# Kernel tuning notes

Hardware: AMD Instinct MI355X
Metric: run time of the kernel (lower is better)

The kernel has to match this reference:

```python
import jax, jax.numpy as jnp
import numpy as np

CONF_THRESH = 0.01
TOP_K = 200        # per-class NMS candidate cap
NMS_THRESH = 0.45
KEEP_TOP_K = 200   # global per-image cap; also output K
TEMPERATURE = 1.0
V0, V1 = 0.1, 0.2  # variances


def _nms_keep(bxs, scs):
    """Greedy NMS over candidates sorted descending by score.
    bxs: [M,4] (x1,y1,x2,y2), scs: [M] (invalid slots have score -1).
    Returns keep mask [M] (bool). Matches torch nm_suppression: a box j is
    suppressed by kept box i iff NOT (IoU(i,j) <= thresh) (NaN IoU suppresses)."""
    x1, y1, x2, y2 = bxs[:, 0], bxs[:, 1], bxs[:, 2], bxs[:, 3]
    area = (x2 - x1) * (y2 - y1)
    xx1 = jnp.maximum(x1[:, None], x1[None, :])
    yy1 = jnp.maximum(y1[:, None], y1[None, :])
    xx2 = jnp.minimum(x2[:, None], x2[None, :])
    yy2 = jnp.minimum(y2[:, None], y2[None, :])
    inter = jnp.clip(xx2 - xx1, 0.0) * jnp.clip(yy2 - yy1, 0.0)
    union = area[None, :] - inter + area[:, None]  # row i: area[i] + area[j] - inter
    iou = inter / union  # [M,M]
    M = scs.shape[0]
    valid = scs > CONF_THRESH

    def step(active, i):
        k_i = active[i]                                  # kept iff still active (sorted desc)
        sup = k_i & jnp.logical_not(iou[i] <= NMS_THRESH)
        return active & jnp.logical_not(sup), k_i

    _, keep = jax.lax.scan(step, valid, jnp.arange(M))
    return keep


def _forward(loc_data, conf_data, dbox_list):
    B, N, C = conf_data.shape
    M, K = TOP_K, KEEP_TOP_K
    # --- box decode (SSD) ---
    db = dbox_list[None]                                   # [1,N,4]
    cxcy = db[..., :2] + loc_data[..., :2] * V0 * db[..., 2:]
    wh = db[..., 2:] * jnp.exp(loc_data[..., 2:] * V1)
    mins = cxcy - wh * 0.5
    boxes = jnp.clip(jnp.concatenate([mins, mins + wh], -1), 0.0, 1.0)  # [B,N,4]
    # --- class scores ---
    probs = jax.nn.softmax(conf_data / TEMPERATURE, axis=-1)
    sc = jnp.swapaxes(probs[..., 1:], 1, 2)                # [B,C-1,N] (skip background)
    masked = jnp.where(sc > CONF_THRESH, sc, -1.0)
    top_sc, top_idx = jax.lax.top_k(masked, M)             # [B,C-1,M] desc
    cand = jnp.take_along_axis(boxes[:, None], top_idx[..., None], axis=2)  # [B,C-1,M,4]
    # --- per-class greedy NMS ---
    keep = jax.vmap(jax.vmap(_nms_keep))(cand, top_sc)     # [B,C-1,M]
    kept_sc = jnp.where(keep, top_sc, 0.0)
    # --- global keep_top_k across classes (torch topk over concatenated dets) ---
    flat = kept_sc.reshape(B, -1)
    order = jnp.argsort(-flat, axis=1)
    rank = jnp.argsort(order, axis=1)                      # inverse permutation = desc rank
    keep_g = (flat > 0.0) & (rank < K)
    fin_sc = jnp.where(keep_g, flat, 0.0).reshape(B, C - 1, M)
    fin_bx = jnp.where(keep_g.reshape(B, C - 1, M)[..., None], cand, 0.0)
    # --- per-class compaction (stable desc sort keeps NMS order among survivors) ---
    ord2 = jnp.argsort(-fin_sc, axis=2)
    sc_out = jnp.take_along_axis(fin_sc, ord2, axis=2)[..., :K]
    bx_out = jnp.take_along_axis(fin_bx, ord2[..., None], axis=2)[..., :K, :]
    body = jnp.concatenate([sc_out[..., None], bx_out], axis=-1)  # [B,C-1,K,5]
    bg = jnp.zeros((B, 1, K, 5), body.dtype)               # class 0 (background) row stays 0
    return jnp.concatenate([bg, body], axis=1)             # [B,C,K,5]


def setup_inputs() -> dict:
    key = jax.random.key(0)
    k1, k2, k3 = jax.random.split(key, 3)
    B, N, C = 8, 32768, 81
    loc_data = jax.random.normal(k1, (B, N, 4), jnp.float32)
    conf_data = jax.random.normal(k2, (B, N, C), jnp.float32)
    dbox_list = jax.random.uniform(k3, (N, 4), jnp.float32, 0.05, 0.95)  # cx,cy,w,h priors
    return {"loc_data": loc_data, "conf_data": conf_data, "dbox_list": dbox_list}


def reference(loc_data, conf_data, dbox_list):
    return _forward(loc_data, conf_data, dbox_list)
```

## Files before the change

kernel.cpp:

```cpp
#include <hip/hip_runtime.h>
#include <stdint.h>

#define CONF_T 0.01f
#define NMS_T  0.45f
#define M_TOP  200
#define TK_BS  512
#define NMS_BS 256
#define TCAP   2048

typedef float float4u __attribute__((ext_vector_type(4), aligned(4)));

__device__ __forceinline__ uint32_t fkey(float f) {
    uint32_t u = __float_as_uint(f);
    return (u & 0x80000000u) ? ~u : (u | 0x80000000u);
}
__device__ __forceinline__ float fkey_inv(uint32_t k) {
    uint32_t u = (k & 0x80000000u) ? (k & 0x7FFFFFFFu) : ~k;
    return __uint_as_float(u);
}

__device__ __forceinline__ void suffix_select(
        uint32_t* hist, uint32_t* wsum, int nb, uint32_t pref, int shift,
        uint32_t wantv, uint32_t* s_prefix, uint32_t* s_want) {
    int tid = threadIdx.x;
    int lane = tid & 63, w = tid >> 6;
    int bpt = nb >> 8;
    int base = tid * bpt;
    uint32_t loc = 0, sfx = 0;
    if (tid < 256) {
        for (int j = 0; j < bpt; j++) loc += hist[base + j];
        sfx = loc;
        #pragma unroll
        for (int d = 1; d < 64; d <<= 1) {
            uint32_t y = __shfl_down(sfx, d);
            if (lane + d < 64) sfx += y;
        }
        if (lane == 0) wsum[w] = sfx;
    }
    __syncthreads();
    if (tid < 256) {
        uint32_t later = 0;
        for (int j = w + 1; j < 4; j++) later += wsum[j];
        uint32_t run = (sfx - loc) + later;
        for (int j = bpt - 1; j >= 0; j--) {
            uint32_t h = hist[base + j];
            uint32_t s2 = run + h;
            if (run < wantv && s2 >= wantv) {
                *s_prefix = pref | ((uint32_t)(base + j) << shift);
                *s_want   = wantv - run;
            }
            run = s2;
        }
    }
    __syncthreads();
}

__device__ __forceinline__ void suffix_select2(
        uint32_t* hist, uint32_t* wsum, int nb, uint32_t want_a, uint32_t want_b,
        uint32_t* s_bin_a, uint32_t* s_bin_b) {
    int tid = threadIdx.x;
    int lane = tid & 63, w = tid >> 6;
    int bpt = nb >> 8;
    int base = tid * bpt;
    uint32_t loc = 0, sfx = 0;
    if (tid < 256) {
        for (int j = 0; j < bpt; j++) loc += hist[base + j];
        sfx = loc;
        #pragma unroll
        for (int d = 1; d < 64; d <<= 1) {
            uint32_t y = __shfl_down(sfx, d);
            if (lane + d < 64) sfx += y;
        }
        if (lane == 0) wsum[w] = sfx;
    }
    __syncthreads();
    if (tid < 256) {
        uint32_t later = 0;
        for (int j = w + 1; j < 4; j++) later += wsum[j];
        uint32_t run = (sfx - loc) + later;
        for (int j = bpt - 1; j >= 0; j--) {
            uint32_t h = hist[base + j];
            uint32_t s2 = run + h;
            if (run < want_a && s2 >= want_a) *s_bin_a = (uint32_t)(base + j);
            if (run < want_b && s2 >= want_b) *s_bin_b = (uint32_t)(base + j);
            run = s2;
        }
    }
    __syncthreads();
}

__device__ __forceinline__ float4 decode_box(float4 l, float4 d) {
    float cx = d.x + (l.x * 0.1f) * d.z;
    float cy = d.y + (l.y * 0.1f) * d.w;
    float w  = d.z * expf(l.z * 0.2f);
    float h  = d.w * expf(l.w * 0.2f);
    float x1 = cx - w * 0.5f, y1 = cy - h * 0.5f;
    float x2 = x1 + w, y2 = y1 + h;
    float4 o;
    o.x = fminf(fmaxf(x1, 0.f), 1.f);
    o.y = fminf(fmaxf(y1, 0.f), 1.f);
    o.z = fminf(fmaxf(x2, 0.f), 1.f);
    o.w = fminf(fmaxf(y2, 0.f), 1.f);
    return o;
}

__global__ __launch_bounds__(256, 4) void softmax_kernel(
        const float* __restrict__ conf, float* __restrict__ sc,
        int* __restrict__ pcnt, int B, int N, int C) {
    int r = blockIdx.x * blockDim.x + threadIdx.x;
    if (r < B) pcnt[r] = 0;
    if (r >= B * N) return;
    const float* p = conf + (size_t)r * 81;
    float v[81];
    #pragma unroll
    for (int i = 0; i < 20; i++) {
        float4u f = *(const float4u*)(p + 4 * i);
        v[4 * i] = f.x; v[4 * i + 1] = f.y; v[4 * i + 2] = f.z; v[4 * i + 3] = f.w;
    }
    v[80] = p[80];
    float m = v[0];
    #pragma unroll
    for (int c = 1; c < 81; c++) m = fmaxf(m, v[c]);
    float s = 0.f;
    #pragma unroll
    for (int c = 0; c < 81; c++) { float e = expf(v[c] - m); v[c] = e; s += e; }
    int b = r / N, n = r % N;
    float* obase = sc + ((size_t)b * (C - 1)) * N + n;
    #pragma unroll
    for (int c = 1; c < 81; c++) obase[(size_t)(c - 1) * N] = v[c] / s;
}

__global__ __launch_bounds__(TK_BS) void sel_kernel(
        const float* __restrict__ sc,
        float* __restrict__ tval, int* __restrict__ tidx,
        int B, int N, int Cm1) {
    const uint32_t KEYN1 = 0x407FFFFFu;
    const uint32_t BIN_N1 = KEYN1 >> 21;
    __shared__ __align__(16) uint32_t hist[2048];
    __shared__ __align__(16) uint32_t tk[TCAP];
    __shared__ int      tix[TCAP];
    __shared__ uint32_t wsum[4];
    __shared__ uint32_t s_prefix, s_want, s_bin_a, s_bin_b;
    __shared__ uint32_t ngt, ntie, tcnt;
    __shared__ float    e_val[256];
    __shared__ int      e_idx[256];
    __shared__ int      tiebuf[256];

    int row = blockIdx.x;
    int tid = threadIdx.x;
    const float* v = sc + (size_t)row * N;
    const float4* v4 = (const float4*)v;
    int n4 = N >> 2;

    bool sampled = (N >= 2048) && ((N & 3) == 0);
    float loF = 0.f, hiF = 0.f;
    if (sampled) {
        int stride = N >> 2;
        float smp[4];
        #pragma unroll
        for (int s = 0; s < 4; s++) smp[s] = v[s * stride + tid];
        for (int i = tid; i < 2048; i += TK_BS) hist[i] = 0;
        __syncthreads();
        #pragma unroll
        for (int s = 0; s < 4; s++) {
            float f = smp[s];
            atomicAdd(&hist[fkey(f > CONF_T ? f : -1.0f) >> 21], 1u);
        }
        __syncthreads();
        suffix_select2(hist, wsum, 2048, 3u, 25u, &s_bin_a, &s_bin_b);
        uint32_t h = s_bin_a, l = s_bin_b;
        uint32_t hi_key = ((h + 1) << 21) - 1u;
        uint32_t lo_key = (l << 21) - 1u;
        hiF = fkey_inv(hi_key);
        loF = fmaxf(fkey_inv(lo_key), CONF_T);
        sampled = (l > BIN_N1);
    }

    if (tid < 256) { e_val[tid] = -1.0f; e_idx[tid] = tid; }
    if (tid == 0) { ngt = 0; ntie = 0; tcnt = 0; }
    __syncthreads();

    bool ok = false;
    uint32_t G = 0, T = 0;
    if (sampled) {
        for (int i0 = tid; i0 < n4; i0 += 16 * TK_BS) {
            float4 f[16];
            #pragma unroll
            for (int u = 0; u < 16; u++) {
                int i = i0 + u * TK_BS;
                if (i < n4) f[u] = v4[i];
            }
            #pragma unroll
            for (int u = 0; u < 16; u++) {
                int i = i0 + u * TK_BS;
                if (i < n4) {
                    float e[4] = { f[u].x, f[u].y, f[u].z, f[u].w };
                    #pragma unroll
                    for (int j = 0; j < 4; j++) {
                        float fv = e[j];
                        if (fv > loF) {
                            int idx = 4 * i + j;
                            if (fv > hiF) {
                                uint32_t p = atomicAdd(&ngt, 1u);
                                if (p < 256) { e_val[p] = fv; e_idx[p] = idx; }
                            } else {
                                uint32_t p = atomicAdd(&tcnt, 1u);
                                if (p < TCAP) { tk[p] = fkey(fv); tix[p] = idx; }
                            }
                        }
                    }
                }
            }
        }
        for (int i = (n4 << 2) + tid; i < N; i += TK_BS) {
            float fv = v[i];
            if (fv > loF) {
                if (fv > hiF) {
                    uint32_t p = atomicAdd(&ngt, 1u);
                    if (p < 256) { e_val[p] = fv; e_idx[p] = i; }
                } else {
                    uint32_t p = atomicAdd(&tcnt, 1u);
                    if (p < TCAP) { tk[p] = fkey(fv); tix[p] = i; }
                }
            }
        }
        __syncthreads();
        G = ngt; T = tcnt;
        ok = (G <= (uint32_t)M_TOP) && (T <= (uint32_t)TCAP) &&
             (G + T >= (uint32_t)M_TOP);
    }

    uint32_t kth = KEYN1, rfin = 0;
    if (ok) {
        uint32_t want_t = (uint32_t)M_TOP - G;
        if (want_t > 0) {
            for (int i = tid; i < 2048; i += TK_BS) hist[i] = 0;
            __syncthreads();
            for (int i = tid; i < (int)T; i += TK_BS) atomicAdd(&hist[tk[i] >> 21], 1u);
            __syncthreads();
            suffix_select(hist, wsum, 2048, 0u, 21, want_t, &s_prefix, &s_want);
            uint32_t pre0 = s_prefix, w0 = s_want;
            uint32_t bb0 = pre0 >> 21;
            for (int i = tid; i < 2048; i += TK_BS) hist[i] = 0;
            __syncthreads();
            for (int i = tid; i < (int)T; i += TK_BS)
                if ((tk[i] >> 21) == bb0) atomicAdd(&hist[(tk[i] >> 10) & 2047u], 1u);
            __syncthreads();
            suffix_select(hist, wsum, 2048, pre0, 10, w0, &s_prefix, &s_want);
            uint32_t pre1 = s_prefix, w1 = s_want;
            for (int i = tid; i < 1024; i += TK_BS) hist[i] = 0;
            __syncthreads();
            for (int i = tid; i < (int)T; i += TK_BS)
                if ((tk[i] >> 10) == (pre1 >> 10)) atomicAdd(&hist[tk[i] & 1023u], 1u);
            __syncthreads();
            suffix_select(hist, wsum, 1024, pre1, 0, w1, &s_prefix, &s_want);
            kth = s_prefix; rfin = s_want;
            for (int i = tid; i < (int)T; i += TK_BS) {
                uint32_t k = tk[i];
                if (k > kth) {
                    uint32_t p = atomicAdd(&ngt, 1u);
                    if (p < 256) { e_val[p] = fkey_inv(k); e_idx[p] = tix[i]; }
                } else if (k == kth) {
                    uint32_t p = atomicAdd(&ntie, 1u);
                    if (p < 256) tiebuf[p] = tix[i];
                }
            }
            __syncthreads();
        }
    } else {
        if (tid < 256) { e_val[tid] = -1.0f; e_idx[tid] = tid; }
        if (tid == 0) { ngt = 0; ntie = 0; tcnt = 0; }
        for (int i = tid; i < 2048; i += TK_BS) hist[i] = 0;
        __syncthreads();
        for (int i = tid; i < n4; i += TK_BS) {
            float4 f = v4[i];
            atomicAdd(&hist[fkey(f.x > CONF_T ? f.x : -1.0f) >> 21], 1u);
            atomicAdd(&hist[fkey(f.y > CONF_T ? f.y : -1.0f) >> 21], 1u);
            atomicAdd(&hist[fkey(f.z > CONF_T ? f.z : -1.0f) >> 21], 1u);
            atomicAdd(&hist[fkey(f.w > CONF_T ? f.w : -1.0f) >> 21], 1u);
        }
        for (int i = (n4 << 2) + tid; i < N; i += TK_BS)
            atomicAdd(&hist[fkey(v[i] > CONF_T ? v[i] : -1.0f) >> 21], 1u);
        __syncthreads();
        suffix_select(hist, wsum, 2048, 0u, 21, M_TOP, &s_prefix, &s_want);
        uint32_t b0 = s_prefix >> 21;
        uint32_t want1 = s_want;
        bool collect_ties = (b0 != BIN_N1);
        for (int i = tid; i < N; i += TK_BS) {
            float f = v[i];
            float mv = f > CONF_T ? f : -1.0f;
            uint32_t k = fkey(mv);
            uint32_t bin = k >> 21;
            if (bin > b0) {
                uint32_t p = atomicAdd(&ngt, 1u);
                if (p < 256) { e_val[p] = mv; e_idx[p] = i; }
            } else if (bin == b0 && collect_ties) {
                uint32_t p = atomicAdd(&tcnt, 1u);
                if (p < TCAP) { tk[p] = k; tix[p] = i; }
            }
        }
        __syncthreads();
        if (collect_ties && tcnt <= TCAP) {
            int Tl = (int)tcnt;
            for (int i = tid; i < 2048; i += TK_BS) hist[i] = 0;
            __syncthreads();
            for (int i = tid; i < Tl; i += TK_BS) atomicAdd(&hist[(tk[i] >> 10) & 2047u], 1u);
            __syncthreads();
            suffix_select(hist, wsum, 2048, b0 << 21, 10, want1, &s_prefix, &s_want);
            uint32_t pre2 = s_prefix; uint32_t want2 = s_want;
            uint32_t b1 = (pre2 >> 10) & 2047u;
            for (int i = tid; i < 1024; i += TK_BS) hist[i] = 0;
            __syncthreads();
            for (int i = tid; i < Tl; i += TK_BS)
                if (((tk[i] >> 10) & 2047u) == b1) atomicAdd(&hist[tk[i] & 1023u], 1u);
            __syncthreads();
            suffix_select(hist, wsum, 1024, pre2, 0, want2, &s_prefix, &s_want);
            kth = s_prefix; rfin = s_want;
            for (int i = tid; i < Tl; i += TK_BS) {
                uint32_t k = tk[i];
                if (k > kth) {
                    uint32_t p = atomicAdd(&ngt, 1u);
                    if (p < 256) { e_val[p] = fkey_inv(k); e_idx[p] = tix[i]; }
                } else if (k == kth) {
                    uint32_t p = atomicAdd(&ntie, 1u);
                    if (p < 256) tiebuf[p] = tix[i];
                }
            }
            __syncthreads();
        } else if (collect_ties) {
            const int shifts[2] = {10, 0};
            const int nbins_[2] = {2048, 1024};
            if (tid == 0) { s_prefix = b0 << 21; s_want = want1; }
            __syncthreads();
            for (int lev = 0; lev < 2; lev++) {
                int shift = shifts[lev];
                int nb = nbins_[lev];
                uint32_t bmask = (uint32_t)nb - 1u;
                uint32_t pref = s_prefix, wantv = s_want;
                uint32_t pmask = 0xFFFFFFFFu << (shift + ((nb == 2048) ? 11 : 10));
                for (int i = tid; i < nb; i += TK_BS) hist[i] = 0;
                __syncthreads();
                for (int i = tid; i < N; i += TK_BS) {
                    float f = v[i];
                    uint32_t k = fkey(f > CONF_T ? f : -1.0f);
                    if ((k & pmask) == (pref & pmask)) atomicAdd(&hist[(k >> shift) & bmask], 1u);
                }
                __syncthreads();
                suffix_select(hist, wsum, nb, pref, shift, wantv, &s_prefix, &s_want);
            }
            kth = s_prefix; rfin = s_want;
            for (int i = tid; i < N; i += TK_BS) {
                float f = v[i];
                float mv = f > CONF_T ? f : -1.0f;
                uint32_t k = fkey(mv);
                if ((k >> 21) == b0) {
                    if (k > kth) {
                        uint32_t p = atomicAdd(&ngt, 1u);
                        if (p < 256) { e_val[p] = mv; e_idx[p] = i; }
                    } else if (k == kth) {
                        uint32_t p = atomicAdd(&ntie, 1u);
                        if (p < 256) tiebuf[p] = i;
                    }
                }
            }
            __syncthreads();
        }
    }

    uint32_t gcount = min(ngt, (uint32_t)M_TOP);
    uint32_t nt = min(ntie, 256u);
    if (tid < (int)nt) {
        int mine = tiebuf[tid];
        uint32_t rk = 0;
        for (uint32_t j = 0; j < nt; j++) if (tiebuf[j] < mine) rk++;
        if (rk < rfin) {
            uint32_t slot = gcount + rk;
            if (slot < M_TOP) { e_val[slot] = fkey_inv(kth); e_idx[slot] = mine; }
        }
    }
    __syncthreads();
    uint64_t* e_pack = (uint64_t*)tk;
    if (tid < 256)
        e_pack[tid] = ((uint64_t)fkey(e_val[tid]) << 32) | (uint32_t)~(uint32_t)e_idx[tid];
    __syncthreads();
    if (tid < M_TOP) {
        uint64_t mine = e_pack[tid];
        uint32_t rk = 0;
        for (int j = 0; j < M_TOP; j++) rk += (e_pack[j] > mine) ? 1u : 0u;
        tval[(size_t)row * M_TOP + rk] = e_val[tid];
        tidx[(size_t)row * M_TOP + rk] = e_idx[tid];
    }
}

__global__ __launch_bounds__(NMS_BS) void nms_kernel(
        const float* __restrict__ tval, const int* __restrict__ tidx,
        const float* __restrict__ loc, const float* __restrict__ dbox,
        float* __restrict__ cand,
        float* __restrict__ cmpval, int* __restrict__ cmpidx,
        int* __restrict__ pcnt,
        int B, int N, int Cm1, int M) {
    __shared__ __align__(16) float4 s_bb[M_TOP];
    __shared__ float    s_ar[M_TOP];
    __shared__ float    s_sc[M_TOP];
    __shared__ __align__(16) uint64_t supT[M_TOP * 4];

    int row = blockIdx.x;
    int b = row / Cm1, c = row % Cm1;
    int tid = threadIdx.x;

    if (tid < M_TOP) {
        float mv = tval[(size_t)row * M_TOP + tid];
        int   mi = tidx[(size_t)row * M_TOP + tid];
        float4 l = ((const float4*)loc)[(size_t)b * N + mi];
        float4 d = ((const float4*)dbox)[mi];
        float4 bx = decode_box(l, d);
        ((float4*)cand)[(size_t)row * M_TOP + tid] = bx;
        s_sc[tid] = mv;
        s_bb[tid] = bx;
        s_ar[tid] = (bx.z - bx.x) * (bx.w - bx.y);
    }
    __syncthreads();

    for (int t = tid; t < M_TOP * 4; t += NMS_BS) {
        int iw = t / M_TOP;
        int j  = t - iw * M_TOP;
        float4 bj = s_bb[j];
        float arJ = s_ar[j];
        int i0 = iw << 6;
        int iN = M_TOP - i0; if (iN > 64) iN = 64; if (iN < 0) iN = 0;
        uint64_t m = 0;
        for (int k = 0; k < iN; k++) {
            float4 bi = s_bb[i0 + k];
            float xx1 = fmaxf(bi.x, bj.x);
            float yy1 = fmaxf(bi.y, bj.y);
            float xx2 = fminf(bi.z, bj.z);
            float yy2 = fminf(bi.w, bj.w);
            float inter = fmaxf(xx2 - xx1, 0.f) * fmaxf(yy2 - yy1, 0.f);
            float uni = (arJ - inter) + s_ar[i0 + k];
            float iou = inter / uni;
            if (!(iou <= NMS_T)) m |= (1ull << k);
        }
        supT[(j << 2) + iw] = m;
    }
    __syncthreads();

    if (tid < 64) {
        int lane = tid;
        uint64_t st0[4], st1[4], st2[4], st3[4];
        bool alive[4]; int keepb[4];
        #pragma unroll
        for (int s = 0; s < 4; s++) {
            int j = (s << 6) + lane;
            bool inb = (j < M_TOP);
            uint64_t w0 = inb ? supT[(j << 2) + 0] : 0ull;
            uint64_t w1 = inb ? supT[(j << 2) + 1] : 0ull;
            uint64_t w2 = inb ? supT[(j << 2) + 2] : 0ull;
            uint64_t w3 = inb ? supT[(j << 2) + 3] : 0ull;
            if (s == 0) { st0[0]=w0; st0[1]=w1; st0[2]=w2; st0[3]=w3; }
            if (s == 1) { st1[0]=w0; st1[1]=w1; st1[2]=w2; st1[3]=w3; }
            if (s == 2) { st2[0]=w0; st2[1]=w1; st2[2]=w2; st2[3]=w3; }
            if (s == 3) { st3[0]=w0; st3[1]=w1; st3[2]=w2; st3[3]=w3; }
            alive[s] = inb ? (s_sc[j] > CONF_T) : false;
            keepb[s] = 0;
        }
        #pragma unroll
        for (int iw = 0; iw < 4; iw++) {
            int lim = M_TOP - (iw << 6); if (lim > 64) lim = 64; if (lim < 0) lim = 0;
            for (int b2 = 0; b2 < lim; b2++) {
                uint64_t mask = __ballot(alive[iw]);
                if ((mask >> b2) & 1ull) {
                    if (lane == b2) keepb[iw] = 1;
                    alive[0] = alive[0] && !((st0[iw] >> b2) & 1ull);
                    alive[1] = alive[1] && !((st1[iw] >> b2) & 1ull);
                    alive[2] = alive[2] && !((st2[iw] >> b2) & 1ull);
                    alive[3] = alive[3] && !((st3[iw] >> b2) & 1ull);
                }
            }
        }
        unsigned long long ball[4];
        int total = 0;
        #pragma unroll
        for (int s = 0; s < 4; s++) { ball[s] = __ballot(keepb[s] != 0); total += (int)__popcll(ball[s]); }
        int base = 0;
        if (lane == 0 && total > 0) base = atomicAdd(&pcnt[b], total);
        base = __shfl(base, 0);
        unsigned long long lower = (lane == 0) ? 0ull : (~0ull >> (64 - lane));
        int off = base;
        #pragma unroll
        for (int s = 0; s < 4; s++) {
            if (keepb[s]) {
                int pos = off + (int)__popcll(ball[s] & lower);
                cmpval[(size_t)b * M + pos] = s_sc[(s << 6) + lane];
                cmpidx[(size_t)b * M + pos] = c * M_TOP + (s << 6) + lane;
            }
            off += (int)__popcll(ball[s]);
        }
    }
}

#define GT_BS 1024
__global__ __launch_bounds__(GT_BS) void gtop_kernel(
        const float* __restrict__ cmpval, const int* __restrict__ cmpidx,
        const int* __restrict__ pcnt, float* __restrict__ gl_val,
        int* __restrict__ gl_idx, int* __restrict__ gl_cnt, int M) {
    int b = blockIdx.x;
    int tid = threadIdx.x;
    int P = pcnt[b];
    const float* cv = cmpval + (size_t)b * M;
    const int*   ci = cmpidx + (size_t)b * M;
    if (P <= M_TOP) {
        for (int i = tid; i < P; i += GT_BS) {
            gl_val[b * M_TOP + i] = cv[i];
            gl_idx[b * M_TOP + i] = ci[i];
        }
        if (tid == 0) gl_cnt[b] = P;
        return;
    }
    __shared__ uint32_t hist[256];
    __shared__ uint32_t s_prefix, s_want;
    __shared__ int tiebuf[256];
    __shared__ uint32_t ntie, wcnt;
    __shared__ int cutoff;
    if (tid == 0) { s_prefix = 0; s_want = M_TOP; }
    for (int pass = 0; pass < 4; pass++) {
        if (tid < 256) hist[tid] = 0;
        __syncthreads();
        uint32_t prefix = s_prefix;
        int shift = 24 - 8 * pass;
        for (int i = tid; i < P; i += GT_BS) {
            uint32_t k = fkey(cv[i]);
            bool ok = (pass == 0) || ((k >> (shift + 8)) == (prefix >> (shift + 8)));
            if (ok) atomicAdd(&hist[(k >> shift) & 255u], 1u);
        }
        __syncthreads();
        if (tid == 0) {
            uint32_t want = s_want, cum = 0; int bin = 0;
            for (int bb = 255; bb >= 0; bb--) {
                if (cum + hist[bb] >= want) { bin = bb; break; }
                cum += hist[bb];
            }
            s_want = want - cum;
            s_prefix = prefix | ((uint32_t)bin << shift);
        }
        __syncthreads();
    }
    uint32_t kth = s_prefix, rfin = s_want;
    if (tid == 0) { ntie = 0; cutoff = -1; wcnt = 0; }
    __syncthreads();
    for (int i = tid; i < P; i += GT_BS) {
        if (fkey(cv[i]) == kth) { uint32_t p = atomicAdd(&ntie, 1u); if (p < 256) tiebuf[p] = ci[i]; }
    }
    __syncthreads();
    uint32_t nt = min(ntie, 256u);
    if (tid < (int)nt) {
        int mine = tiebuf[tid];
        uint32_t rk = 0;
        for (uint32_t j = 0; j < nt; j++) if (tiebuf[j] < mine) rk++;
        if (rk == rfin - 1) cutoff = mine;
    }
    __syncthreads();
    int cut = cutoff;
    for (int i = tid; i < P; i += GT_BS) {
        uint32_t k = fkey(cv[i]);
        if (k > kth || (k == kth && ci[i] <= cut)) {
            uint32_t p = atomicAdd(&wcnt, 1u);
            gl_val[b * M_TOP + p] = cv[i];
            gl_idx[b * M_TOP + p] = ci[i];
        }
    }
    if (tid == 0) gl_cnt[b] = M_TOP;
}

__global__ __launch_bounds__(256) void out_kernel(
        const float* __restrict__ gl_val, const int* __restrict__ gl_idx,
        const int* __restrict__ gl_cnt, const float* __restrict__ cand,
        float* __restrict__ out, int C, int Cm1) {
    int row = blockIdx.x;
    int b = row / C, cc = row % C;
    int tid = threadIdx.x;
    size_t oslab = (size_t)row * M_TOP * 5;
    if (cc == 0) {
        float4 z; z.x = 0.f; z.y = 0.f; z.z = 0.f; z.w = 0.f;
        float4* o4 = (float4*)(out + oslab);
        for (int i = tid; i < M_TOP * 5 / 4; i += 256) o4[i] = z;
        return;
    }
    int c = cc - 1;
    __shared__ float lv[M_TOP];
    __shared__ int   lm[M_TOP];
    __shared__ uint32_t nloc;
    if (tid == 0) nloc = 0;
    __syncthreads();
    int cnt = gl_cnt[b];
    for (int i = tid; i < cnt; i += 256) {
        int idx = gl_idx[b * M_TOP + i];
        if (idx / M_TOP == c) {
            uint32_t p = atomicAdd(&nloc, 1u);
            lv[p] = gl_val[b * M_TOP + i];
            lm[p] = idx % M_TOP;
        }
    }
    __syncthreads();
    int nc = (int)nloc;
    if (tid < M_TOP) {
        if (tid < nc) {
            float v = lv[tid]; int m = lm[tid];
            int rk = 0;
            for (int j = 0; j < nc; j++)
                if (lv[j] > v || (lv[j] == v && lm[j] < m)) rk++;
            float4 bb = ((const float4*)cand)[((size_t)(b * Cm1 + c)) * M_TOP + m];
            size_t o = oslab + (size_t)rk * 5;
            out[o] = v; out[o + 1] = bb.x; out[o + 2] = bb.y;
            out[o + 3] = bb.z; out[o + 4] = bb.w;
        } else {
            size_t o = oslab + (size_t)tid * 5;
            out[o] = 0.f; out[o + 1] = 0.f; out[o + 2] = 0.f;
            out[o + 3] = 0.f; out[o + 4] = 0.f;
        }
    }
}

extern "C" void kernel_launch(void* const* d_in, const int* in_sizes, int n_in,
                              void* d_out, int out_size, void* d_ws, size_t ws_size,
                              hipStream_t stream) {
    const float* loc  = (const float*)d_in[0];
    const float* conf = (const float*)d_in[1];
    const float* dbox = (const float*)d_in[2];
    int N   = in_sizes[2] / 4;
    int B   = in_sizes[0] / (4 * N);
    int C   = in_sizes[1] / (B * N);
    int Cm1 = C - 1;
    int M   = Cm1 * M_TOP;

    char* ws = (char*)d_ws;
    size_t off = 0;
    auto alloc = [&](size_t bytes) -> char* {
        char* p = ws + off;
        off = (off + bytes + 255) & ~(size_t)255;
        return p;
    };
    float* sc     = (float*)alloc((size_t)B * Cm1 * N * sizeof(float));
    float* cand   = (float*)alloc((size_t)B * M * 4 * sizeof(float));
    int*   pcnt   = (int*)alloc((size_t)B * sizeof(int));
    float* cmpval = (float*)alloc((size_t)B * M * sizeof(float));
    int*   cmpidx = (int*)alloc((size_t)B * M * sizeof(int));
    float* gl_val = (float*)alloc((size_t)B * M_TOP * sizeof(float));
    int*   gl_idx = (int*)alloc((size_t)B * M_TOP * sizeof(int));
    int*   gl_cnt = (int*)alloc((size_t)B * sizeof(int));
    float* tval   = (float*)alloc((size_t)B * Cm1 * M_TOP * sizeof(float));
    int*   tidx   = (int*)alloc((size_t)B * Cm1 * M_TOP * sizeof(int));

    int bn = B * N;
    softmax_kernel<<<(bn + 255) / 256, 256, 0, stream>>>(conf, sc, pcnt, B, N, C);
    sel_kernel<<<B * Cm1, TK_BS, 0, stream>>>(sc, tval, tidx, B, N, Cm1);
    nms_kernel<<<B * Cm1, NMS_BS, 0, stream>>>(tval, tidx, loc, dbox, cand,
                                               cmpval, cmpidx, pcnt, B, N, Cm1, M);
    gtop_kernel<<<B, GT_BS, 0, stream>>>(cmpval, cmpidx, pcnt, gl_val, gl_idx, gl_cnt, M);
    out_kernel<<<B * C, 256, 0, stream>>>(gl_val, gl_idx, gl_cnt, cand, (float*)d_out, C, Cm1);
}
```

Measured before the change: 278.7 us.

## Replace materialized softmax+per-class top-k with sampled-threshold streaming selection

Instead of writing the full [B,C-1,N] softmax matrix and running a radix select over each row, the code samples 2048 anchors per image to estimate per-class score thresholds. It then streams conf once, recomputing softmax and using a log-domain quick reject to collect only candidates above the threshold into small per-row buffers. A finish kernel resolves the exact top-200 from those buffers and falls back to a full recompute when the estimate fails. The NMS IoU mask now computes only the lower-triangular entries, and gtop uses the parallel suffix_select. The aim is to remove the large score-matrix write and re-read, at the cost of added complexity, atomics and a slow fallback path.

```diff
diff --git a/kernel.cpp b/kernel.cpp
--- a/kernel.cpp
+++ b/kernel.cpp
@@ -6,7 +6,11 @@
 #define M_TOP  200
 #define TK_BS  512
 #define NMS_BS 256
+#define FIN_BS 512
 #define TCAP   2048
+#define GCAP   256
+#define KEYN1  0x407FFFFFu
+#define BIN_N1 (KEYN1 >> 21)
 
 typedef float float4u __attribute__((ext_vector_type(4), aligned(4)));
 
@@ -24,7 +28,7 @@
         uint32_t wantv, uint32_t* s_prefix, uint32_t* s_want) {
     int tid = threadIdx.x;
     int lane = tid & 63, w = tid >> 6;
-    int bpt = nb >> 8;
+    int bpt = nb >> 8; if (bpt < 1) bpt = 1;
     int base = tid * bpt;
     uint32_t loc = 0, sfx = 0;
     if (tid < 256) {
@@ -104,6 +108,356 @@
     return o;
 }
 
+__device__ __forceinline__ void softmax_ms(const float* __restrict__ p,
+                                           float& m_out, float& s_out) {
+    float m;
+    {
+        float4u f = *(const float4u*)p;
+        m = f.x; m = fmaxf(m, f.y); m = fmaxf(m, f.z); m = fmaxf(m, f.w);
+        #pragma unroll
+        for (int i = 1; i < 20; i++) {
+            float4u g = *(const float4u*)(p + 4 * i);
+            m = fmaxf(m, g.x); m = fmaxf(m, g.y); m = fmaxf(m, g.z); m = fmaxf(m, g.w);
+        }
+        m = fmaxf(m, p[80]);
+    }
+    float s = 0.f;
+    #pragma unroll
+    for (int i = 0; i < 20; i++) {
+        float4u g = *(const float4u*)(p + 4 * i);
+        s += expf(g.x - m); s += expf(g.y - m); s += expf(g.z - m); s += expf(g.w - m);
+    }
+    s += expf(p[80] - m);
+    m_out = m; s_out = s;
+}
+
+__global__ __launch_bounds__(256) void samp_kernel(
+        const float* __restrict__ conf, float* __restrict__ samp, int N, int Cm1) {
+    int b = blockIdx.x >> 3;
+    int t = ((blockIdx.x & 7) << 8) + threadIdx.x;
+    int n = (t >> 9) * (N >> 2) + (t & 511);
+    const float* p = conf + ((size_t)b * N + n) * 81;
+    float m, s; softmax_ms(p, m, s);
+    float* ob = samp + ((size_t)b * Cm1) * 2048 + t;
+    #pragma unroll
+    for (int i = 0; i < 20; i++) {
+        float4u g = *(const float4u*)(p + 4 * i);
+        float e4[4] = { g.x, g.y, g.z, g.w };
+        #pragma unroll
+        for (int j = 0; j < 4; j++) {
+            int c = 4 * i + j;
+            if (c >= 1) ob[(size_t)(c - 1) * 2048] = expf(e4[j] - m) / s;
+        }
+    }
+    ob[(size_t)(Cm1 - 1) * 2048] = expf(p[80] - m) / s;
+}
+
+__global__ __launch_bounds__(TK_BS) void thr_kernel(
+        const float* __restrict__ samp, float* __restrict__ thrLo,
+        float* __restrict__ thrHi, uint32_t* __restrict__ gcnt,
+        uint32_t* __restrict__ tcnt, int* __restrict__ pcnt, int Cm1) {
+    __shared__ uint32_t hist[2048];
+    __shared__ uint32_t wsum[4];
+    __shared__ uint32_t s_bin_a, s_bin_b;
+    int row = blockIdx.x, tid = threadIdx.x;
+    const float* sp = samp + ((size_t)row << 11);
+    for (int i = tid; i < 2048; i += TK_BS) hist[i] = 0;
+    __syncthreads();
+    for (int i = tid; i < 2048; i += TK_BS) {
+        float f = sp[i];
+        atomicAdd(&hist[fkey(f > CONF_T ? f : -1.0f) >> 21], 1u);
+    }
+    __syncthreads();
+    suffix_select2(hist, wsum, 2048, 3u, 25u, &s_bin_a, &s_bin_b);
+    if (tid == 0) {
+        uint32_t h = s_bin_a, l = s_bin_b;
+        uint32_t hi_key = ((h + 1) << 21) - 1u;
+        uint32_t lo_key = (l << 21) - 1u;
+        float hiF = fkey_inv(hi_key);
+        float loF = fmaxf(fkey_inv(lo_key), CONF_T);
+        bool rok = (l > BIN_N1);
+        thrLo[row] = rok ? loF : __uint_as_float(0x7F800000u);
+        thrHi[row] = hiF;
+        gcnt[row] = 0; tcnt[row] = 0;
+        if ((row % Cm1) == 0) pcnt[row / Cm1] = 0;
+    }
+}
+
+__global__ __launch_bounds__(256) void fsel_kernel(
+        const float* __restrict__ conf,
+        const float* __restrict__ thrLo, const float* __restrict__ thrHi,
+        float* __restrict__ gval, int* __restrict__ gidx, uint32_t* __restrict__ gcnt,
+        uint32_t* __restrict__ tkey, int* __restrict__ tixg, uint32_t* __restrict__ tcnt,
+        int N, int Cm1) {
+    __shared__ float s_lo[128], s_hi[128], s_ln[128];
+    int nb = N >> 8;
+    int b = blockIdx.x / nb;
+    int n = ((blockIdx.x % nb) << 8) + threadIdx.x;
+    if (threadIdx.x < Cm1) {
+        float lo = thrLo[b * Cm1 + threadIdx.x];
+        s_lo[threadIdx.x] = lo;
+        s_hi[threadIdx.x] = thrHi[b * Cm1 + threadIdx.x];
+        s_ln[threadIdx.x] = logf(lo);
+    }
+    __syncthreads();
+    const float* p = conf + ((size_t)b * N + n) * 81;
+    float m, s; softmax_ms(p, m, s);
+    float t0m = m + logf(s) - 1e-3f;
+    int lane = threadIdx.x & 63;
+    uint64_t lowerm = (lane == 0) ? 0ull : (~0ull >> (64 - lane));
+    int rowb = b * Cm1;
+
+    auto proc = [&](int c, float x) {
+        bool quick = x > (t0m + s_ln[c - 1]);
+        uint64_t mq = __ballot(quick);
+        if (mq == 0) return;
+        float fv = 0.f; bool ex = false, hb = false;
+        if (quick) {
+            fv = expf(x - m) / s;
+            ex = fv > s_lo[c - 1];
+            hb = ex && (fv > s_hi[c - 1]);
+        }
+        uint64_t mhi = __ballot(hb);
+        uint64_t mlo = __ballot(ex && !hb);
+        int row = rowb + (c - 1);
+        if (mhi) {
+            int src = (int)__ffsll((unsigned long long)mhi) - 1;
+            uint32_t bse = 0;
+            if (lane == src) bse = atomicAdd(&gcnt[row], (uint32_t)__popcll(mhi));
+            bse = (uint32_t)__shfl((int)bse, src);
+            if (hb) {
+                uint32_t pp = bse + (uint32_t)__popcll(mhi & lowerm);
+                if (pp < GCAP) {
+                    gval[(size_t)row * GCAP + pp] = fv;
+                    gidx[(size_t)row * GCAP + pp] = n;
+                }
+            }
+        }
+        if (mlo) {
+            int src = (int)__ffsll((unsigned long long)mlo) - 1;
+            uint32_t bse = 0;
+            if (lane == src) bse = atomicAdd(&tcnt[row], (uint32_t)__popcll(mlo));
+            bse = (uint32_t)__shfl((int)bse, src);
+            if (ex && !hb) {
+                uint32_t pp = bse + (uint32_t)__popcll(mlo & lowerm);
+                if (pp < TCAP) {
+                    tkey[(size_t)row * TCAP + pp] = fkey(fv);
+                    tixg[(size_t)row * TCAP + pp] = n;
+                }
+            }
+        }
+    };
+
+    {
+        float4u g = *(const float4u*)p;
+        proc(1, g.y); proc(2, g.z); proc(3, g.w);
+    }
+    for (int i = 1; i < 20; i++) {
+        float4u g = *(const float4u*)(p + 4 * i);
+        proc(4 * i, g.x); proc(4 * i + 1, g.y); proc(4 * i + 2, g.z); proc(4 * i + 3, g.w);
+    }
+    proc(80, p[80]);
+}
+
+__global__ __launch_bounds__(FIN_BS) void fin_kernel(
+        const float* __restrict__ conf,
+        const float* __restrict__ thrLo,
+        const float* __restrict__ gval, const int* __restrict__ gidx,
+        const uint32_t* __restrict__ gcnt,
+        const uint32_t* __restrict__ tkeyg, const int* __restrict__ tixg2,
+        const uint32_t* __restrict__ tcntg,
+        float* __restrict__ tval, int* __restrict__ tidx,
+        int N, int Cm1) {
+    __shared__ __align__(16) uint32_t hist[2048];
+    __shared__ __align__(16) uint32_t tk[TCAP];
+    __shared__ int      tix[TCAP];
+    __shared__ uint32_t wsum[4];
+    __shared__ uint32_t s_prefix, s_want;
+    __shared__ uint32_t ngt, ntie, tcs;
+    __shared__ float    e_val[256];
+    __shared__ int      e_idx[256];
+    __shared__ int      tiebuf[256];
+
+    int row = blockIdx.x, tid = threadIdx.x;
+    int b = row / Cm1, cls = (row % Cm1) + 1;
+    uint32_t G = gcnt[row], T = tcntg[row];
+    bool ok = (thrLo[row] < 2.0f) && (G <= (uint32_t)M_TOP) &&
+              (T <= (uint32_t)TCAP) && (G + T >= (uint32_t)M_TOP);
+
+    if (tid < 256) { e_val[tid] = -1.0f; e_idx[tid] = tid; }
+    if (tid == 0) { ngt = 0; ntie = 0; tcs = 0; }
+    __syncthreads();
+
+    uint32_t kth = KEYN1, rfin = 0;
+    if (ok) {
+        if (tid < (int)G) {
+            e_val[tid] = gval[(size_t)row * GCAP + tid];
+            e_idx[tid] = gidx[(size_t)row * GCAP + tid];
+        }
+        for (int i = tid; i < (int)T; i += FIN_BS) {
+            tk[i]  = tkeyg[(size_t)row * TCAP + i];
+            tix[i] = tixg2[(size_t)row * TCAP + i];
+        }
+        if (tid == 0) ngt = G;
+        __syncthreads();
+        uint32_t want_t = (uint32_t)M_TOP - G;
+        if (want_t > 0) {
+            for (int i = tid; i < 2048; i += FIN_BS) hist[i] = 0;
+            __syncthreads();
+            for (int i = tid; i < (int)T; i += FIN_BS) atomicAdd(&hist[tk[i] >> 21], 1u);
+            __syncthreads();
+            suffix_select(hist, wsum, 2048, 0u, 21, want_t, &s_prefix, &s_want);
+            uint32_t pre0 = s_prefix, w0 = s_want;
+            uint32_t bb0 = pre0 >> 21;
+            for (int i = tid; i < 2048; i += FIN_BS) hist[i] = 0;
+            __syncthreads();
+            for (int i = tid; i < (int)T; i += FIN_BS)
+                if ((tk[i] >> 21) == bb0) atomicAdd(&hist[(tk[i] >> 10) & 2047u], 1u);
+            __syncthreads();
+            suffix_select(hist, wsum, 2048, pre0, 10, w0, &s_prefix, &s_want);
+            uint32_t pre1 = s_prefix, w1 = s_want;
+            for (int i = tid; i < 1024; i += FIN_BS) hist[i] = 0;
+            __syncthreads();
+            for (int i = tid; i < (int)T; i += FIN_BS)
+                if ((tk[i] >> 10) == (pre1 >> 10)) atomicAdd(&hist[tk[i] & 1023u], 1u);
+            __syncthreads();
+            suffix_select(hist, wsum, 1024, pre1, 0, w1, &s_prefix, &s_want);
+            kth = s_prefix; rfin = s_want;
+            for (int i = tid; i < (int)T; i += FIN_BS) {
+                uint32_t k = tk[i];
+                if (k > kth) {
+                    uint32_t pq = atomicAdd(&ngt, 1u);
+                    if (pq < 256) { e_val[pq] = fkey_inv(k); e_idx[pq] = tix[i]; }
+                } else if (k == kth) {
+                    uint32_t pq = atomicAdd(&ntie, 1u);
+                    if (pq < 256) tiebuf[pq] = tix[i];
+                }
+            }
+            __syncthreads();
+        }
+    } else {
+        auto probf = [&](int i) -> float {
+            const float* pp = conf + ((size_t)b * N + i) * 81;
+            float mm, ss; softmax_ms(pp, mm, ss);
+            return expf(pp[cls] - mm) / ss;
+        };
+        for (int i = tid; i < 2048; i += FIN_BS) hist[i] = 0;
+        __syncthreads();
+        for (int i = tid; i < N; i += FIN_BS) {
+            float f = probf(i);
+            atomicAdd(&hist[fkey(f > CONF_T ? f : -1.0f) >> 21], 1u);
+        }
+        __syncthreads();
+        suffix_select(hist, wsum, 2048, 0u, 21, (uint32_t)M_TOP, &s_prefix, &s_want);
+        uint32_t b0 = s_prefix >> 21;
+        uint32_t want1 = s_want;
+        bool collect = (b0 != BIN_N1);
+        for (int i = tid; i < N; i += FIN_BS) {
+            float f = probf(i);
+            float mv = f > CONF_T ? f : -1.0f;
+            uint32_t k = fkey(mv);
+            uint32_t bin = k >> 21;
+            if (bin > b0) {
+                uint32_t pq = atomicAdd(&ngt, 1u);
+                if (pq < 256) { e_val[pq] = mv; e_idx[pq] = i; }
+            } else if (bin == b0 && collect) {
+                uint32_t pq = atomicAdd(&tcs, 1u);
+                if (pq < TCAP) { tk[pq] = k; tix[pq] = i; }
+            }
+        }
+        __syncthreads();
+        if (collect && tcs <= TCAP) {
+            int Tl = (int)tcs;
+            for (int i = tid; i < 2048; i += FIN_BS) hist[i] = 0;
+            __syncthreads();
+            for (int i = tid; i < Tl; i += FIN_BS) atomicAdd(&hist[(tk[i] >> 10) & 2047u], 1u);
+            __syncthreads();
+            suffix_select(hist, wsum, 2048, b0 << 21, 10, want1, &s_prefix, &s_want);
+            uint32_t pre2 = s_prefix, want2 = s_want;
+            uint32_t b1 = (pre2 >> 10) & 2047u;
+            for (int i = tid; i < 1024; i += FIN_BS) hist[i] = 0;
+            __syncthreads();
+            for (int i = tid; i < Tl; i += FIN_BS)
+                if (((tk[i] >> 10) & 2047u) == b1) atomicAdd(&hist[tk[i] & 1023u], 1u);
+            __syncthreads();
+            suffix_select(hist, wsum, 1024, pre2, 0, want2, &s_prefix, &s_want);
+            kth = s_prefix; rfin = s_want;
+            for (int i = tid; i < Tl; i += FIN_BS) {
+                uint32_t k = tk[i];
+                if (k > kth) {
+                    uint32_t pq = atomicAdd(&ngt, 1u);
+                    if (pq < 256) { e_val[pq] = fkey_inv(k); e_idx[pq] = tix[i]; }
+                } else if (k == kth) {
+                    uint32_t pq = atomicAdd(&ntie, 1u);
+                    if (pq < 256) tiebuf[pq] = tix[i];
+                }
+            }
+            __syncthreads();
+        } else if (collect) {
+            const int shifts[2] = {10, 0};
+            const int nbins_[2] = {2048, 1024};
+            if (tid == 0) { s_prefix = b0 << 21; s_want = want1; }
+            __syncthreads();
+            for (int lev = 0; lev < 2; lev++) {
+                int shift = shifts[lev];
+                int nbv = nbins_[lev];
+                uint32_t bmask = (uint32_t)nbv - 1u;
+                uint32_t pref = s_prefix, wantv = s_want;
+                uint32_t pmask = 0xFFFFFFFFu << (shift + ((nbv == 2048) ? 11 : 10));
+                for (int i = tid; i < nbv; i += FIN_BS) hist[i] = 0;
+                __syncthreads();
+                for (int i = tid; i < N; i += FIN_BS) {
+                    float f = probf(i);
+                    uint32_t k = fkey(f > CONF_T ? f : -1.0f);
+                    if ((k & pmask) == (pref & pmask)) atomicAdd(&hist[(k >> shift) & bmask], 1u);
+                }
+                __syncthreads();
+                suffix_select(hist, wsum, nbv, pref, shift, wantv, &s_prefix, &s_want);
+            }
+            kth = s_prefix; rfin = s_want;
+            for (int i = tid; i < N; i += FIN_BS) {
+                float f = probf(i);
+                float mv = f > CONF_T ? f : -1.0f;
+                uint32_t k = fkey(mv);
+                if ((k >> 21) == b0) {
+                    if (k > kth) {
+                        uint32_t pq = atomicAdd(&ngt, 1u);
+                        if (pq < 256) { e_val[pq] = mv; e_idx[pq] = i; }
+                    } else if (k == kth) {
+                        uint32_t pq = atomicAdd(&ntie, 1u);
+                        if (pq < 256) tiebuf[pq] = i;
+                    }
+                }
+            }
+            __syncthreads();
+        }
+    }
+
+    uint32_t gcount = min(ngt, (uint32_t)M_TOP);
+    uint32_t nt = min(ntie, 256u);
+    if (tid < (int)nt) {
+        int mine = tiebuf[tid];
+        uint32_t rk = 0;
+        for (uint32_t j = 0; j < nt; j++) if (tiebuf[j] < mine) rk++;
+        if (rk < rfin) {
+            uint32_t slot = gcount + rk;
+            if (slot < M_TOP) { e_val[slot] = fkey_inv(kth); e_idx[slot] = mine; }
+        }
+    }
+    __syncthreads();
+    uint64_t* e_pack = (uint64_t*)tk;
+    if (tid < 256)
+        e_pack[tid] = ((uint64_t)fkey(e_val[tid]) << 32) | (uint32_t)~(uint32_t)e_idx[tid];
+    __syncthreads();
+    if (tid < M_TOP) {
+        uint64_t mine = e_pack[tid];
+        uint32_t rk = 0;
+        for (int j = 0; j < M_TOP; j++) rk += (e_pack[j] > mine) ? 1u : 0u;
+        tval[(size_t)row * M_TOP + rk] = e_val[tid];
+        tidx[(size_t)row * M_TOP + rk] = e_idx[tid];
+    }
+}
+
 __global__ __launch_bounds__(256, 4) void softmax_kernel(
         const float* __restrict__ conf, float* __restrict__ sc,
         int* __restrict__ pcnt, int B, int N, int C) {
@@ -134,8 +488,6 @@
         const float* __restrict__ sc,
         float* __restrict__ tval, int* __restrict__ tidx,
         int B, int N, int Cm1) {
-    const uint32_t KEYN1 = 0x407FFFFFu;
-    const uint32_t BIN_N1 = KEYN1 >> 21;
     __shared__ __align__(16) uint32_t hist[2048];
     __shared__ __align__(16) uint32_t tk[TCAP];
     __shared__ int      tix[TCAP];
@@ -424,23 +776,25 @@
     for (int t = tid; t < M_TOP * 4; t += NMS_BS) {
         int iw = t / M_TOP;
         int j  = t - iw * M_TOP;
-        float4 bj = s_bb[j];
-        float arJ = s_ar[j];
         int i0 = iw << 6;
-        int iN = M_TOP - i0; if (iN > 64) iN = 64; if (iN < 0) iN = 0;
-        uint64_t m = 0;
-        for (int k = 0; k < iN; k++) {
-            float4 bi = s_bb[i0 + k];
-            float xx1 = fmaxf(bi.x, bj.x);
-            float yy1 = fmaxf(bi.y, bj.y);
-            float xx2 = fminf(bi.z, bj.z);
-            float yy2 = fminf(bi.w, bj.w);
-            float inter = fmaxf(xx2 - xx1, 0.f) * fmaxf(yy2 - yy1, 0.f);
-            float uni = (arJ - inter) + s_ar[i0 + k];
-            float iou = inter / uni;
-            if (!(iou <= NMS_T)) m |= (1ull << k);
-        }
-        supT[(j << 2) + iw] = m;
+        uint64_t mm = 0;
+        int iN = j - i0; if (iN > 64) iN = 64;
+        if (iN > 0) {
+            float4 bj = s_bb[j];
+            float arJ = s_ar[j];
+            for (int k = 0; k < iN; k++) {
+                float4 bi = s_bb[i0 + k];
+                float xx1 = fmaxf(bi.x, bj.x);
+                float yy1 = fmaxf(bi.y, bj.y);
+                float xx2 = fminf(bi.z, bj.z);
+                float yy2 = fminf(bi.w, bj.w);
+                float inter = fmaxf(xx2 - xx1, 0.f) * fmaxf(yy2 - yy1, 0.f);
+                float uni = (arJ - inter) + s_ar[i0 + k];
+                float iou = inter / uni;
+                if (!(iou <= NMS_T)) mm |= (1ull << k);
+            }
+        }
+        supT[(j << 2) + iw] = mm;
     }
     __syncthreads();
 
@@ -517,6 +871,7 @@
         return;
     }
     __shared__ uint32_t hist[256];
+    __shared__ uint32_t wsum[4];
     __shared__ uint32_t s_prefix, s_want;
     __shared__ int tiebuf[256];
     __shared__ uint32_t ntie, wcnt;
@@ -529,20 +884,12 @@
         int shift = 24 - 8 * pass;
         for (int i = tid; i < P; i += GT_BS) {
             uint32_t k = fkey(cv[i]);
-            bool ok = (pass == 0) || ((k >> (shift + 8)) == (prefix >> (shift + 8)));
-            if (ok) atomicAdd(&hist[(k >> shift) & 255u], 1u);
-        }
-        __syncthreads();
-        if (tid == 0) {
-            uint32_t want = s_want, cum = 0; int bin = 0;
-            for (int bb = 255; bb >= 0; bb--) {
-                if (cum + hist[bb] >= want) { bin = bb; break; }
-                cum += hist[bb];
-            }
-            s_want = want - cum;
-            s_prefix = prefix | ((uint32_t)bin << shift);
-        }
-        __syncthreads();
+            bool okm = (pass == 0) || ((k >> (shift + 8)) == (prefix >> (shift + 8)));
+            if (okm) atomicAdd(&hist[(k >> shift) & 255u], 1u);
+        }
+        __syncthreads();
+        uint32_t wantv = s_want;
+        suffix_select(hist, wsum, 256, prefix, shift, wantv, &s_prefix, &s_want);
     }
     uint32_t kth = s_prefix, rfin = s_want;
     if (tid == 0) { ntie = 0; cutoff = -1; wcnt = 0; }
@@ -631,6 +978,7 @@
     int C   = in_sizes[1] / (B * N);
     int Cm1 = C - 1;
     int M   = Cm1 * M_TOP;
+    int R   = B * Cm1;
 
     char* ws = (char*)d_ws;
     size_t off = 0;
@@ -639,7 +987,6 @@
         off = (off + bytes + 255) & ~(size_t)255;
         return p;
     };
-    float* sc     = (float*)alloc((size_t)B * Cm1 * N * sizeof(float));
     float* cand   = (float*)alloc((size_t)B * M * 4 * sizeof(float));
     int*   pcnt   = (int*)alloc((size_t)B * sizeof(int));
     float* cmpval = (float*)alloc((size_t)B * M * sizeof(float));
@@ -647,14 +994,36 @@
     float* gl_val = (float*)alloc((size_t)B * M_TOP * sizeof(float));
     int*   gl_idx = (int*)alloc((size_t)B * M_TOP * sizeof(int));
     int*   gl_cnt = (int*)alloc((size_t)B * sizeof(int));
-    float* tval   = (float*)alloc((size_t)B * Cm1 * M_TOP * sizeof(float));
-    int*   tidx   = (int*)alloc((size_t)B * Cm1 * M_TOP * sizeof(int));
-
-    int bn = B * N;
-    softmax_kernel<<<(bn + 255) / 256, 256, 0, stream>>>(conf, sc, pcnt, B, N, C);
-    sel_kernel<<<B * Cm1, TK_BS, 0, stream>>>(sc, tval, tidx, B, N, Cm1);
-    nms_kernel<<<B * Cm1, NMS_BS, 0, stream>>>(tval, tidx, loc, dbox, cand,
-                                               cmpval, cmpidx, pcnt, B, N, Cm1, M);
+    float* tval   = (float*)alloc((size_t)R * M_TOP * sizeof(float));
+    int*   tidx   = (int*)alloc((size_t)R * M_TOP * sizeof(int));
+
+    bool fast = (N >= 2048) && ((N & 255) == 0);
+    if (fast) {
+        float*    samp  = (float*)alloc((size_t)R * 2048 * sizeof(float));
+        float*    thrLo = (float*)alloc((size_t)R * sizeof(float));
+        float*    thrHi = (float*)alloc((size_t)R * sizeof(float));
+        uint32_t* gcnt  = (uint32_t*)alloc((size_t)R * sizeof(uint32_t));
+        uint32_t* tcnt  = (uint32_t*)alloc((size_t)R * sizeof(uint32_t));
+        float*    gvalb = (float*)alloc((size_t)R * GCAP * sizeof(float));
+        int*      gidxb = (int*)alloc((size_t)R * GCAP * sizeof(int));
+        uint32_t* tkeyb = (uint32_t*)alloc((size_t)R * TCAP * sizeof(uint32_t));
+        int*      tixgb = (int*)alloc((size_t)R * TCAP * sizeof(int));
+
+        samp_kernel<<<B * 8, 256, 0, stream>>>(conf, samp, N, Cm1);
+        thr_kernel<<<R, TK_BS, 0, stream>>>(samp, thrLo, thrHi, gcnt, tcnt, pcnt, Cm1);
+        fsel_kernel<<<B * (N >> 8), 256, 0, stream>>>(conf, thrLo, thrHi,
+                                                      gvalb, gidxb, gcnt,
+                                                      tkeyb, tixgb, tcnt, N, Cm1);
+        fin_kernel<<<R, FIN_BS, 0, stream>>>(conf, thrLo, gvalb, gidxb, gcnt,
+                                             tkeyb, tixgb, tcnt, tval, tidx, N, Cm1);
+    } else {
+        float* sc = (float*)alloc((size_t)B * Cm1 * N * sizeof(float));
+        int bn = B * N;
+        softmax_kernel<<<(bn + 255) / 256, 256, 0, stream>>>(conf, sc, pcnt, B, N, C);
+        sel_kernel<<<R, TK_BS, 0, stream>>>(sc, tval, tidx, B, N, Cm1);
+    }
+    nms_kernel<<<R, NMS_BS, 0, stream>>>(tval, tidx, loc, dbox, cand,
+                                         cmpval, cmpidx, pcnt, B, N, Cm1, M);
     gtop_kernel<<<B, GT_BS, 0, stream>>>(cmpval, cmpidx, pcnt, gl_val, gl_idx, gl_cnt, M);
     out_kernel<<<B * C, 256, 0, stream>>>(gl_val, gl_idx, gl_cnt, cand, (float*)d_out, C, Cm1);
 }
```

New measurement: 491.5 us. +76.4%, slower.
